# Performance work log

Hardware: AMD Instinct MI355X
Metric: run time of the kernel (lower is better)

The kernel has to match this reference:

```python
import jax, jax.numpy as jnp
import numpy as np


def _lstm_layer(x, h0, c0, W_ih, W_hh, b_ih, b_hh):
    # x: [B,T,D], h0/c0: [B,H], W_ih: [4H,D], W_hh: [4H,H]
    # Precompute input contribution for all timesteps (one big GEMM).
    xg = jnp.einsum('btd,gd->btg', x, W_ih) + (b_ih + b_hh)  # [B,T,4H]

    def step(carry, xg_t):
        h, c = carry
        g = xg_t + h @ W_hh.T  # [B,4H]
        i, f, gg, o = jnp.split(g, 4, axis=-1)  # torch gate order: i,f,g,o
        i = jax.nn.sigmoid(i)
        f = jax.nn.sigmoid(f)
        gg = jnp.tanh(gg)
        o = jax.nn.sigmoid(o)
        c = f * c + i * gg
        h = o * jnp.tanh(c)
        return (h, c), h

    (hT, cT), hs = jax.lax.scan(step, (h0, c0), jnp.swapaxes(xg, 0, 1))
    return jnp.swapaxes(hs, 0, 1), hT, cT  # [B,T,H], [B,H], [B,H]


def setup_inputs() -> dict:
    key = jax.random.key(0)
    ks = jax.random.split(key, 20)
    B, T, D, H, O = 32, 2048, 64, 256, 32
    s = 0.05
    return {
        'inputs': jax.random.normal(ks[0], (B, T, D), jnp.float32),
        'h0': jax.random.normal(ks[1], (2, B, H), jnp.float32) * s,
        'c0': jax.random.normal(ks[2], (2, B, H), jnp.float32) * s,
        'W_ih0': jax.random.normal(ks[3], (4 * H, D), jnp.float32) * s,
        'W_hh0': jax.random.normal(ks[4], (4 * H, H), jnp.float32) * s,
        'b_ih0': jax.random.normal(ks[5], (4 * H,), jnp.float32) * s,
        'b_hh0': jax.random.normal(ks[6], (4 * H,), jnp.float32) * s,
        'W_ih1': jax.random.normal(ks[7], (4 * H, H), jnp.float32) * s,
        'W_hh1': jax.random.normal(ks[8], (4 * H, H), jnp.float32) * s,
        'b_ih1': jax.random.normal(ks[9], (4 * H,), jnp.float32) * s,
        'b_hh1': jax.random.normal(ks[10], (4 * H,), jnp.float32) * s,
        'W_d0': jax.random.normal(ks[11], (H, H), jnp.float32) * s,
        'b_d0': jax.random.normal(ks[12], (H,), jnp.float32) * s,
        'W_d1': jax.random.normal(ks[13], (H, H), jnp.float32) * s,
        'b_d1': jax.random.normal(ks[14], (H,), jnp.float32) * s,
        'W_out': jax.random.normal(ks[15], (O, H), jnp.float32) * s,
        'b_out': jax.random.normal(ks[16], (O,), jnp.float32) * s,
    }


def reference(inputs, h0, c0, W_ih0, W_hh0, b_ih0, b_hh0,
              W_ih1, W_hh1, b_ih1, b_hh1,
              W_d0, b_d0, W_d1, b_d1, W_out, b_out):
    # Stacked 2-layer LSTM (batch_first) matching torch nn.LSTM.
    y0, h_0, c_0 = _lstm_layer(inputs, h0[0], c0[0], W_ih0, W_hh0, b_ih0, b_hh0)
    y1, h_1, c_1 = _lstm_layer(y0, h0[1], c0[1], W_ih1, W_hh1, b_ih1, b_hh1)
    h_n = jnp.stack([h_0, h_1], axis=0)
    c_n = jnp.stack([c_0, c_1], axis=0)
    # Dense head: two Linear+ReLU, then output Linear.
    d = jax.nn.relu(jnp.einsum('bth,oh->bto', y1, W_d0) + b_d0)
    d = jax.nn.relu(jnp.einsum('bth,oh->bto', d, W_d1) + b_d1)
    out = jnp.einsum('bth,oh->bto', d, W_out) + b_out
    return out, h_n, c_n
```

## Files before the change

kernel.cpp:

```cpp
#include <hip/hip_runtime.h>
#include <hip/hip_bf16.h>
#include <cstddef>
#include <cstdint>

#define BB 32
#define TT 2048
#define DD 64
#define HH 256
#define OO 32
#define NBLK 8

#define OUT_ELEMS (BB*TT*OO)
#define HN_OFF OUT_ELEMS
#define CN_OFF (HN_OFF + 2*BB*HH)

#define O_XBF   ((size_t)0)
#define O_H0    ((size_t)8388608)
#define O_XH1   ((size_t)41959424)
#define O_WP0   ((size_t)109101056)
#define O_WP1   ((size_t)109756416)
#define O_B0    ((size_t)110804992)
#define O_B1    ((size_t)110809088)
#define O_WD0T  ((size_t)110813184)
#define O_WD1T  ((size_t)111075328)
#define O_WOUT  ((size_t)111337472)
#define O_D0    ((size_t)111370240)
#define O_D1    (O_D0 + 256)

typedef short short8 __attribute__((ext_vector_type(8)));
typedef float f32x4 __attribute__((ext_vector_type(4)));

__device__ __forceinline__ float sigm_(float x){ return 1.0f/(1.0f+__expf(-x)); }
__device__ __forceinline__ float tanhf_(float x){
    float xc = fminf(fmaxf(x, -15.0f), 15.0f);
    float e = __expf(2.0f*xc);
    return (e-1.0f)/(e+1.0f);
}
__device__ __forceinline__ unsigned short f2bf(float f){
    __hip_bfloat16 h = __float2bfloat16(f);
    return *reinterpret_cast<unsigned short*>(&h);
}
__device__ __forceinline__ unsigned int pack2(float a, float b){
    return (unsigned int)f2bf(a) | ((unsigned int)f2bf(b) << 16);
}
__device__ __forceinline__ short8 ld8(const unsigned short* p){
    return *reinterpret_cast<const short8*>(p);
}

__device__ __forceinline__ void pollLine(const int* flags, int tgt, int lane){
    int it = 0;
    while (true) {
        int v = tgt;
        if (lane < NBLK)
            v = __hip_atomic_load(flags + lane, __ATOMIC_RELAXED, __HIP_MEMORY_SCOPE_AGENT);
        if (__all(v >= tgt)) break;
        if (++it > (1<<18)) break;
    }
    asm volatile("" ::: "memory");
}

__global__ void prep_kernel(const float* __restrict__ x, const float* __restrict__ h0,
    const float* __restrict__ Wih0, const float* __restrict__ Whh0,
    const float* __restrict__ bih0, const float* __restrict__ bhh0,
    const float* __restrict__ Wih1, const float* __restrict__ Whh1,
    const float* __restrict__ bih1, const float* __restrict__ bhh1,
    const float* __restrict__ Wd0, const float* __restrict__ Wd1,
    const float* __restrict__ Wout, char* __restrict__ ws)
{
    int i = blockIdx.x*256 + threadIdx.x;
    if (i < 4194304) {
        int t = i >> 11, rem = i & 2047, b = rem >> 6, d = rem & 63;
        ((unsigned short*)(ws+O_XBF))[i] = f2bf(x[(size_t)b*131072 + t*64 + d]);
        return;
    }
    i -= 4194304;
    if (i < 327680) {
        int R = i / 320, k = i - R*320;
        int lrow = R & 15, s = (R>>4)&1, hr = (R>>5)&3, jj = R>>7;
        int gate = 2*s + (lrow>>3);
        int h = 32*jj + 8*hr + (lrow&7);
        int src = 256*gate + h;
        float v = (k < 64) ? Wih0[src*64 + k] : Whh0[src*256 + (k-64)];
        ((unsigned short*)(ws+O_WP0))[i] = f2bf(v);
        return;
    }
    i -= 327680;
    if (i < 524288) {
        int R = i >> 9, k = i & 511;
        int lrow = R & 15, s = (R>>4)&1, hr = (R>>5)&3, jj = R>>7;
        int gate = 2*s + (lrow>>3);
        int h = 32*jj + 8*hr + (lrow&7);
        int src = 256*gate + h;
        float v = (k < 256) ? Wih1[src*256 + k] : Whh1[src*256 + (k-256)];
        ((unsigned short*)(ws+O_WP1))[i] = f2bf(v);
        return;
    }
    i -= 524288;
    if (i < 1024) { ((float*)(ws+O_B0))[i] = bih0[i] + bhh0[i]; return; }
    i -= 1024;
    if (i < 1024) { ((float*)(ws+O_B1))[i] = bih1[i] + bhh1[i]; return; }
    i -= 1024;
    if (i < 8192) { ((unsigned short*)(ws+O_H0))[i] = f2bf(h0[i]); return; }
    i -= 8192;
    if (i < 8192) {
        int b = i >> 8, h = i & 255;
        ((unsigned short*)(ws+O_XH1))[b*512 + 256 + h] = f2bf(h0[8192 + i]);
        return;
    }
    i -= 8192;
    if (i < 65536) { int o = i & 255, h = i >> 8; ((float*)(ws+O_WD0T))[i] = Wd0[o*256 + h]; return; }
    i -= 65536;
    if (i < 65536) { int o = i & 255, h = i >> 8; ((float*)(ws+O_WD1T))[i] = Wd1[o*256 + h]; return; }
    i -= 65536;
    if (i < 8192) { int o = i & 31, h = i >> 5; ((float*)(ws+O_WOUT))[i] = Wout[o*256 + h]; return; }
    i -= 8192;
    if (i < 4096) { ((int*)(ws+O_D0))[i] = 0; return; }
}

template<int L>
__device__ void lstm_body(int j, char* ws, const float* __restrict__ c0_in,
                          float* __restrict__ out)
{
    constexpr int KK  = L ? 512 : 320;
    constexpr int NKT = KK / 32;

    const int tid  = threadIdx.x;
    const int wv   = tid >> 6;
    const int lane = tid & 63;
    const int bh   = wv >> 2;
    const int hr   = wv & 3;
    const int lrow = lane & 15;
    const int q    = lane >> 4;
    const int koff = q * 8;
    const int qe   = q & 1;
    const int fb   = bh*16 + lrow;
    const int hbase= 32*j + 8*hr + 4*qe;
    const bool lo  = (lane < 32);

    const unsigned short* Wp = (const unsigned short*)(ws + (L ? O_WP1 : O_WP0));
    const float* bias = (const float*)(ws + (L ? O_B1 : O_B0));

    const int wavebase = (j*4 + hr) * 32;
    short8 a0[NKT], a1[NKT];
#pragma unroll
    for (int kk = 0; kk < NKT; ++kk) {
        a0[kk] = ld8(Wp + (size_t)(wavebase +      lrow)*KK + kk*32 + koff);
        a1[kk] = ld8(Wp + (size_t)(wavebase + 16 + lrow)*KK + kk*32 + koff);
    }

    float bi[4], bf_[4], bg[4], bo[4], c[4], hv[4];
#pragma unroll
    for (int r = 0; r < 4; ++r) {
        int hg = hbase + r;
        bi[r] = bias[hg];       bf_[r] = bias[256+hg];
        bg[r] = bias[512+hg];   bo[r]  = bias[768+hg];
        c[r]  = c0_in[(size_t)L*8192 + fb*256 + hg];
        hv[r] = 0.f;
    }

    int* flags0 = (int*)(ws + O_D0);
    int* flags1 = (int*)(ws + O_D1);
    int* myflag = (L ? flags1 : flags0) + j;

    const unsigned short* xb = (const unsigned short*)(ws + O_XBF) + fb*64  + koff;
    const unsigned short* hb = (const unsigned short*)(ws + O_H0)  + fb*256 + koff;
    const unsigned short* xh = (const unsigned short*)(ws + O_XH1) + fb*512 + koff;

    unsigned long long* stA;
    unsigned long long* stB = nullptr;
    if (L == 0) {
        stA = (unsigned long long*)((unsigned short*)(ws + O_H0)  + (size_t)8192 + fb*256 + hbase);
        stB = (unsigned long long*)((unsigned short*)(ws + O_XH1) + (size_t)fb*512 + hbase);
    } else {
        stA = (unsigned long long*)((unsigned short*)(ws + O_XH1) + (size_t)16384 + fb*512 + 256 + hbase);
    }

    for (int t = 0; t < TT; ++t) {
        f32x4 A0 = {0.f,0.f,0.f,0.f}, A1 = {0.f,0.f,0.f,0.f};

        if (L == 0) {
            short8 bx0 = ld8(xb), bx1 = ld8(xb + 32);
            A0 = __builtin_amdgcn_mfma_f32_16x16x32_bf16(a0[0], bx0, A0, 0,0,0);
            A1 = __builtin_amdgcn_mfma_f32_16x16x32_bf16(a1[0], bx0, A1, 0,0,0);
            A0 = __builtin_amdgcn_mfma_f32_16x16x32_bf16(a0[1], bx1, A0, 0,0,0);
            A1 = __builtin_amdgcn_mfma_f32_16x16x32_bf16(a1[1], bx1, A1, 0,0,0);

            pollLine(flags0, t, lane);

            short8 b[8];
#pragma unroll
            for (int kk = 0; kk < 8; ++kk) b[kk] = ld8(hb + 32*kk);
#pragma unroll
            for (int kk = 0; kk < 8; ++kk) {
                A0 = __builtin_amdgcn_mfma_f32_16x16x32_bf16(a0[2+kk], b[kk], A0, 0,0,0);
                A1 = __builtin_amdgcn_mfma_f32_16x16x32_bf16(a1[2+kk], b[kk], A1, 0,0,0);
            }
        } else {
            pollLine(flags0, t+1, lane);
            short8 b[8];
#pragma unroll
            for (int kk = 0; kk < 8; ++kk) b[kk] = ld8(xh + 32*kk);
#pragma unroll
            for (int kk = 0; kk < 8; ++kk) {
                A0 = __builtin_amdgcn_mfma_f32_16x16x32_bf16(a0[kk], b[kk], A0, 0,0,0);
                A1 = __builtin_amdgcn_mfma_f32_16x16x32_bf16(a1[kk], b[kk], A1, 0,0,0);
            }
            pollLine(flags1, t, lane);
#pragma unroll
            for (int kk = 0; kk < 8; ++kk) b[kk] = ld8(xh + 256 + 32*kk);
#pragma unroll
            for (int kk = 0; kk < 8; ++kk) {
                A0 = __builtin_amdgcn_mfma_f32_16x16x32_bf16(a0[8+kk], b[kk], A0, 0,0,0);
                A1 = __builtin_amdgcn_mfma_f32_16x16x32_bf16(a1[8+kk], b[kk], A1, 0,0,0);
            }
        }

#pragma unroll
        for (int r = 0; r < 4; ++r) {
            float x0 = A0[r], y0 = __shfl_xor(x0, 32, 64);
            float x1 = A1[r], y1 = __shfl_xor(x1, 32, 64);
            float gi = (lo ? x0 : y0) + bi[r];
            float gf = (lo ? y0 : x0) + bf_[r];
            float gg = (lo ? x1 : y1) + bg[r];
            float go = (lo ? y1 : x1) + bo[r];
            float iv = sigm_(gi), fv = sigm_(gf), gv = tanhf_(gg), ov = sigm_(go);
            c[r]  = fv*c[r] + iv*gv;
            hv[r] = ov * tanhf_(c[r]);
        }

        unsigned long long w =
            (unsigned long long)pack2(hv[0], hv[1]) |
            ((unsigned long long)pack2(hv[2], hv[3]) << 32);

        if (L == 0) {
            if (lo) __hip_atomic_store(stA, w, __ATOMIC_RELAXED, __HIP_MEMORY_SCOPE_AGENT);
            else    __hip_atomic_store(stB, w, __ATOMIC_RELAXED, __HIP_MEMORY_SCOPE_AGENT);
        } else {
            if (lo) __hip_atomic_store(stA, w, __ATOMIC_RELAXED, __HIP_MEMORY_SCOPE_AGENT);
        }

        __syncthreads();
        if (tid == 0)
            __hip_atomic_store(myflag, t+1, __ATOMIC_RELAXED, __HIP_MEMORY_SCOPE_AGENT);

        xb += 2048; hb += 8192; xh += 16384;
        stA += (L ? 4096 : 2048);
        if (L == 0) stB += 4096;
    }

    if (lo) {
#pragma unroll
        for (int r = 0; r < 4; ++r) {
            out[HN_OFF + (size_t)L*8192 + fb*256 + hbase + r] = hv[r];
            out[CN_OFF + (size_t)L*8192 + fb*256 + hbase + r] = c[r];
        }
    }
}

__global__ __launch_bounds__(512, 2) void lstm_fused(char* ws,
                                                     const float* __restrict__ c0_in,
                                                     float* __restrict__ out)
{
    if (blockIdx.x < NBLK) lstm_body<0>(blockIdx.x, ws, c0_in, out);
    else                   lstm_body<1>(blockIdx.x - NBLK, ws, c0_in, out);
}

__global__ __launch_bounds__(256) void head_kernel(const char* __restrict__ ws,
    const float* __restrict__ bd0, const float* __restrict__ bd1,
    const float* __restrict__ bout, float* __restrict__ out)
{
    const __hip_bfloat16* xh1 = (const __hip_bfloat16*)(ws + O_XH1);
    const float* Wd0T  = (const float*)(ws + O_WD0T);
    const float* Wd1T  = (const float*)(ws + O_WD1T);
    const float* WoutT = (const float*)(ws + O_WOUT);

    __shared__ float buf0[16][256];
    __shared__ float buf1[16][256];
    const int row0 = blockIdx.x * 16;
    const int tid = threadIdx.x;

#pragma unroll
    for (int i = 0; i < 16; ++i) {
        int r = row0 + i;
        int b = r >> 11, t = r & 2047;
        buf0[i][tid] = __bfloat162float(xh1[(size_t)(t+1)*16384 + b*512 + 256 + tid]);
    }
    __syncthreads();

    {
        float acc[16];
        float bv = bd0[tid];
#pragma unroll
        for (int r = 0; r < 16; ++r) acc[r] = bv;
        for (int h = 0; h < 256; ++h) {
            float w = Wd0T[h*256 + tid];
#pragma unroll
            for (int r = 0; r < 16; ++r) acc[r] += w * buf0[r][h];
        }
        __syncthreads();
#pragma unroll
        for (int r = 0; r < 16; ++r) buf1[r][tid] = fmaxf(acc[r], 0.0f);
    }
    __syncthreads();

    {
        float acc[16];
        float bv = bd1[tid];
#pragma unroll
        for (int r = 0; r < 16; ++r) acc[r] = bv;
        for (int h = 0; h < 256; ++h) {
            float w = Wd1T[h*256 + tid];
#pragma unroll
            for (int r = 0; r < 16; ++r) acc[r] += w * buf1[r][h];
        }
        __syncthreads();
#pragma unroll
        for (int r = 0; r < 16; ++r) buf0[r][tid] = fmaxf(acc[r], 0.0f);
    }
    __syncthreads();

    {
        const int o = tid & 31;
        const int rr = tid >> 5;
        float a0 = bout[o], a1 = bout[o];
        for (int h = 0; h < 256; ++h) {
            float w = WoutT[h*32 + o];
            a0 += w * buf0[rr*2 + 0][h];
            a1 += w * buf0[rr*2 + 1][h];
        }
        out[(size_t)(row0 + rr*2 + 0)*32 + o] = a0;
        out[(size_t)(row0 + rr*2 + 1)*32 + o] = a1;
    }
}

extern "C" void kernel_launch(void* const* d_in, const int* in_sizes, int n_in,
                              void* d_out, int out_size, void* d_ws, size_t ws_size,
                              hipStream_t stream) {
    const float* x    = (const float*)d_in[0];
    const float* h0   = (const float*)d_in[1];
    const float* c0   = (const float*)d_in[2];
    const float* Wih0 = (const float*)d_in[3];
    const float* Whh0 = (const float*)d_in[4];
    const float* bih0 = (const float*)d_in[5];
    const float* bhh0 = (const float*)d_in[6];
    const float* Wih1 = (const float*)d_in[7];
    const float* Whh1 = (const float*)d_in[8];
    const float* bih1 = (const float*)d_in[9];
    const float* bhh1 = (const float*)d_in[10];
    const float* Wd0  = (const float*)d_in[11];
    const float* bd0  = (const float*)d_in[12];
    const float* Wd1  = (const float*)d_in[13];
    const float* bd1  = (const float*)d_in[14];
    const float* Wout = (const float*)d_in[15];
    const float* bout = (const float*)d_in[16];

    char* ws = (char*)d_ws;
    float* out = (float*)d_out;

    prep_kernel<<<20344, 256, 0, stream>>>(x, h0, Wih0, Whh0, bih0, bhh0,
                                           Wih1, Whh1, bih1, bhh1,
                                           Wd0, Wd1, Wout, ws);
    lstm_fused<<<2*NBLK, 512, 0, stream>>>(ws, c0, out);
    head_kernel<<<4096, 256, 0, stream>>>(ws, bd0, bd1, bout, out);
}
```

Measured before the change: 12.42 ms.

## Replace per-step flag barriers with tagged hidden-state words for dataflow sync

Each hidden-state element is now stored as a 32-bit word holding the bf16 value and a timestep tag. Consumers spin on the tags of the data they actually read, so the per-step __syncthreads plus flag store/poll round trip is gone. The input x is read and converted to bf16 inside the recurrent loop, which removes the prep pass over x. The cost is double the storage and bandwidth for hidden states and a 134MB memset on every call to clear the tags.

```diff
diff --git a/kernel.cpp b/kernel.cpp
--- a/kernel.cpp
+++ b/kernel.cpp
@@ -14,21 +14,21 @@
 #define HN_OFF OUT_ELEMS
 #define CN_OFF (HN_OFF + 2*BB*HH)
 
-#define O_XBF   ((size_t)0)
-#define O_H0    ((size_t)8388608)
-#define O_XH1   ((size_t)41959424)
-#define O_WP0   ((size_t)109101056)
-#define O_WP1   ((size_t)109756416)
-#define O_B0    ((size_t)110804992)
-#define O_B1    ((size_t)110809088)
-#define O_WD0T  ((size_t)110813184)
-#define O_WD1T  ((size_t)111075328)
-#define O_WOUT  ((size_t)111337472)
-#define O_D0    ((size_t)111370240)
-#define O_D1    (O_D0 + 256)
+#define O_H0T   ((size_t)0)
+#define O_H1T   ((size_t)67141632)
+#define TAGBYTES ((size_t)134283264)
+#define O_WP0   ((size_t)134283264)
+#define O_WP1   ((size_t)134938624)
+#define O_B0    ((size_t)135987200)
+#define O_B1    ((size_t)135991296)
+#define O_WD0T  ((size_t)135995392)
+#define O_WD1T  ((size_t)136257536)
+#define O_WOUT  ((size_t)136519680)
 
 typedef short short8 __attribute__((ext_vector_type(8)));
 typedef float f32x4 __attribute__((ext_vector_type(4)));
+typedef unsigned int uint4v __attribute__((ext_vector_type(4)));
+typedef unsigned long long ull;
 
 __device__ __forceinline__ float sigm_(float x){ return 1.0f/(1.0f+__expf(-x)); }
 __device__ __forceinline__ float tanhf_(float x){
@@ -40,26 +40,59 @@
     __hip_bfloat16 h = __float2bfloat16(f);
     return *reinterpret_cast<unsigned short*>(&h);
 }
-__device__ __forceinline__ unsigned int pack2(float a, float b){
-    return (unsigned int)f2bf(a) | ((unsigned int)f2bf(b) << 16);
-}
 __device__ __forceinline__ short8 ld8(const unsigned short* p){
     return *reinterpret_cast<const short8*>(p);
 }
 
-__device__ __forceinline__ void pollLine(const int* flags, int tgt, int lane){
+__device__ __forceinline__ short8 packtile(uint4v a, uint4v b){
+    uint4v u;
+    u.x = (a.y & 0xffff0000u) | (a.x >> 16);
+    u.y = (a.w & 0xffff0000u) | (a.z >> 16);
+    u.z = (b.y & 0xffff0000u) | (b.x >> 16);
+    u.w = (b.w & 0xffff0000u) | (b.z >> 16);
+    return __builtin_bit_cast(short8, u);
+}
+__device__ __forceinline__ short8 cvt8(float4 a, float4 b){
+    uint4v u;
+    u.x = ((unsigned)f2bf(a.y)<<16) | f2bf(a.x);
+    u.y = ((unsigned)f2bf(a.w)<<16) | f2bf(a.z);
+    u.z = ((unsigned)f2bf(b.y)<<16) | f2bf(b.x);
+    u.w = ((unsigned)f2bf(b.w)<<16) | f2bf(b.z);
+    return __builtin_bit_cast(short8, u);
+}
+
+__device__ __forceinline__ void validate8(const unsigned int* base,
+                                          uint4v* va, uint4v* vb, unsigned tg)
+{
     int it = 0;
     while (true) {
-        int v = tgt;
-        if (lane < NBLK)
-            v = __hip_atomic_load(flags + lane, __ATOMIC_RELAXED, __HIP_MEMORY_SCOPE_AGENT);
-        if (__all(v >= tgt)) break;
-        if (++it > (1<<18)) break;
-    }
-    asm volatile("" ::: "memory");
-}
-
-__global__ void prep_kernel(const float* __restrict__ x, const float* __restrict__ h0,
+        unsigned bad = 0;
+#pragma unroll
+        for (int kk = 0; kk < 8; ++kk) {
+            unsigned m = ((va[kk].x ^ tg) | (va[kk].z ^ tg) |
+                          (vb[kk].x ^ tg) | (vb[kk].z ^ tg)) & 0xffffu;
+            if (m) bad |= 1u << kk;
+        }
+        if (bad == 0) return;
+#pragma unroll
+        for (int kk = 0; kk < 8; ++kk) {
+            if (bad & (1u << kk)) {
+                const ull* p = (const ull*)(base + kk*32);
+                ull u0 = __hip_atomic_load(p+0, __ATOMIC_RELAXED, __HIP_MEMORY_SCOPE_AGENT);
+                ull u1 = __hip_atomic_load(p+1, __ATOMIC_RELAXED, __HIP_MEMORY_SCOPE_AGENT);
+                ull u2 = __hip_atomic_load(p+2, __ATOMIC_RELAXED, __HIP_MEMORY_SCOPE_AGENT);
+                ull u3 = __hip_atomic_load(p+3, __ATOMIC_RELAXED, __HIP_MEMORY_SCOPE_AGENT);
+                va[kk].x = (unsigned)u0; va[kk].y = (unsigned)(u0>>32);
+                va[kk].z = (unsigned)u1; va[kk].w = (unsigned)(u1>>32);
+                vb[kk].x = (unsigned)u2; vb[kk].y = (unsigned)(u2>>32);
+                vb[kk].z = (unsigned)u3; vb[kk].w = (unsigned)(u3>>32);
+            }
+        }
+        if (++it > 4096) return;
+    }
+}
+
+__global__ void prep_kernel(const float* __restrict__ h0,
     const float* __restrict__ Wih0, const float* __restrict__ Whh0,
     const float* __restrict__ bih0, const float* __restrict__ bhh0,
     const float* __restrict__ Wih1, const float* __restrict__ Whh1,
@@ -68,12 +101,6 @@
     const float* __restrict__ Wout, char* __restrict__ ws)
 {
     int i = blockIdx.x*256 + threadIdx.x;
-    if (i < 4194304) {
-        int t = i >> 11, rem = i & 2047, b = rem >> 6, d = rem & 63;
-        ((unsigned short*)(ws+O_XBF))[i] = f2bf(x[(size_t)b*131072 + t*64 + d]);
-        return;
-    }
-    i -= 4194304;
     if (i < 327680) {
         int R = i / 320, k = i - R*320;
         int lrow = R & 15, s = (R>>4)&1, hr = (R>>5)&3, jj = R>>7;
@@ -100,11 +127,13 @@
     i -= 1024;
     if (i < 1024) { ((float*)(ws+O_B1))[i] = bih1[i] + bhh1[i]; return; }
     i -= 1024;
-    if (i < 8192) { ((unsigned short*)(ws+O_H0))[i] = f2bf(h0[i]); return; }
+    if (i < 8192) {
+        ((unsigned int*)(ws+O_H0T))[i] = ((unsigned)f2bf(h0[i])<<16) | 1u;
+        return;
+    }
     i -= 8192;
     if (i < 8192) {
-        int b = i >> 8, h = i & 255;
-        ((unsigned short*)(ws+O_XH1))[b*512 + 256 + h] = f2bf(h0[8192 + i]);
+        ((unsigned int*)(ws+O_H1T))[i] = ((unsigned)f2bf(h0[8192+i])<<16) | 1u;
         return;
     }
     i -= 8192;
@@ -113,13 +142,11 @@
     if (i < 65536) { int o = i & 255, h = i >> 8; ((float*)(ws+O_WD1T))[i] = Wd1[o*256 + h]; return; }
     i -= 65536;
     if (i < 8192) { int o = i & 31, h = i >> 5; ((float*)(ws+O_WOUT))[i] = Wout[o*256 + h]; return; }
-    i -= 8192;
-    if (i < 4096) { ((int*)(ws+O_D0))[i] = 0; return; }
 }
 
 template<int L>
-__device__ void lstm_body(int j, char* ws, const float* __restrict__ c0_in,
-                          float* __restrict__ out)
+__device__ void lstm_body(int j, char* ws, const float* __restrict__ xin,
+                          const float* __restrict__ c0_in, float* __restrict__ out)
 {
     constexpr int KK  = L ? 512 : 320;
     constexpr int NKT = KK / 32;
@@ -158,60 +185,71 @@
         hv[r] = 0.f;
     }
 
-    int* flags0 = (int*)(ws + O_D0);
-    int* flags1 = (int*)(ws + O_D1);
-    int* myflag = (L ? flags1 : flags0) + j;
-
-    const unsigned short* xb = (const unsigned short*)(ws + O_XBF) + fb*64  + koff;
-    const unsigned short* hb = (const unsigned short*)(ws + O_H0)  + fb*256 + koff;
-    const unsigned short* xh = (const unsigned short*)(ws + O_XH1) + fb*512 + koff;
-
-    unsigned long long* stA;
-    unsigned long long* stB = nullptr;
-    if (L == 0) {
-        stA = (unsigned long long*)((unsigned short*)(ws + O_H0)  + (size_t)8192 + fb*256 + hbase);
-        stB = (unsigned long long*)((unsigned short*)(ws + O_XH1) + (size_t)fb*512 + hbase);
-    } else {
-        stA = (unsigned long long*)((unsigned short*)(ws + O_XH1) + (size_t)16384 + fb*512 + 256 + hbase);
-    }
+    const unsigned int* h0t = (const unsigned int*)(ws + O_H0T);
+    const unsigned int* h1t = (const unsigned int*)(ws + O_H1T);
+    unsigned int* dst = (unsigned int*)(ws + (L ? O_H1T : O_H0T));
+    const size_t laneoff = (size_t)fb*256 + koff;
 
     for (int t = 0; t < TT; ++t) {
         f32x4 A0 = {0.f,0.f,0.f,0.f}, A1 = {0.f,0.f,0.f,0.f};
 
         if (L == 0) {
-            short8 bx0 = ld8(xb), bx1 = ld8(xb + 32);
+            const float4* xp4 = (const float4*)(xin + ((size_t)fb*TT + t)*64 + koff);
+            float4 x0 = xp4[0], x1 = xp4[1];
+            float4 x2 = xp4[8], x3 = xp4[9];
+
+            const unsigned int* hp = h0t + (size_t)t*8192 + laneoff;
+            uint4v va[8], vb[8];
+#pragma unroll
+            for (int kk = 0; kk < 8; ++kk) {
+                va[kk] = *(const uint4v*)(hp + kk*32);
+                vb[kk] = *(const uint4v*)(hp + kk*32 + 4);
+            }
+            short8 bx0 = cvt8(x0, x1), bx1 = cvt8(x2, x3);
             A0 = __builtin_amdgcn_mfma_f32_16x16x32_bf16(a0[0], bx0, A0, 0,0,0);
             A1 = __builtin_amdgcn_mfma_f32_16x16x32_bf16(a1[0], bx0, A1, 0,0,0);
             A0 = __builtin_amdgcn_mfma_f32_16x16x32_bf16(a0[1], bx1, A0, 0,0,0);
             A1 = __builtin_amdgcn_mfma_f32_16x16x32_bf16(a1[1], bx1, A1, 0,0,0);
 
-            pollLine(flags0, t, lane);
-
-            short8 b[8];
-#pragma unroll
-            for (int kk = 0; kk < 8; ++kk) b[kk] = ld8(hb + 32*kk);
+            validate8(hp, va, vb, (unsigned)(t+1));
 #pragma unroll
             for (int kk = 0; kk < 8; ++kk) {
-                A0 = __builtin_amdgcn_mfma_f32_16x16x32_bf16(a0[2+kk], b[kk], A0, 0,0,0);
-                A1 = __builtin_amdgcn_mfma_f32_16x16x32_bf16(a1[2+kk], b[kk], A1, 0,0,0);
+                short8 bfr = packtile(va[kk], vb[kk]);
+                A0 = __builtin_amdgcn_mfma_f32_16x16x32_bf16(a0[2+kk], bfr, A0, 0,0,0);
+                A1 = __builtin_amdgcn_mfma_f32_16x16x32_bf16(a1[2+kk], bfr, A1, 0,0,0);
             }
         } else {
-            pollLine(flags0, t+1, lane);
-            short8 b[8];
-#pragma unroll
-            for (int kk = 0; kk < 8; ++kk) b[kk] = ld8(xh + 32*kk);
-#pragma unroll
-            for (int kk = 0; kk < 8; ++kk) {
-                A0 = __builtin_amdgcn_mfma_f32_16x16x32_bf16(a0[kk], b[kk], A0, 0,0,0);
-                A1 = __builtin_amdgcn_mfma_f32_16x16x32_bf16(a1[kk], b[kk], A1, 0,0,0);
+            {
+                const unsigned int* ap = h0t + (size_t)(t+1)*8192 + laneoff;
+                uint4v va[8], vb[8];
+#pragma unroll
+                for (int kk = 0; kk < 8; ++kk) {
+                    va[kk] = *(const uint4v*)(ap + kk*32);
+                    vb[kk] = *(const uint4v*)(ap + kk*32 + 4);
+                }
+                validate8(ap, va, vb, (unsigned)(t+2));
+#pragma unroll
+                for (int kk = 0; kk < 8; ++kk) {
+                    short8 bfr = packtile(va[kk], vb[kk]);
+                    A0 = __builtin_amdgcn_mfma_f32_16x16x32_bf16(a0[kk], bfr, A0, 0,0,0);
+                    A1 = __builtin_amdgcn_mfma_f32_16x16x32_bf16(a1[kk], bfr, A1, 0,0,0);
+                }
             }
-            pollLine(flags1, t, lane);
-#pragma unroll
-            for (int kk = 0; kk < 8; ++kk) b[kk] = ld8(xh + 256 + 32*kk);
-#pragma unroll
-            for (int kk = 0; kk < 8; ++kk) {
-                A0 = __builtin_amdgcn_mfma_f32_16x16x32_bf16(a0[8+kk], b[kk], A0, 0,0,0);
-                A1 = __builtin_amdgcn_mfma_f32_16x16x32_bf16(a1[8+kk], b[kk], A1, 0,0,0);
+            {
+                const unsigned int* bp = h1t + (size_t)t*8192 + laneoff;
+                uint4v va[8], vb[8];
+#pragma unroll
+                for (int kk = 0; kk < 8; ++kk) {
+                    va[kk] = *(const uint4v*)(bp + kk*32);
+                    vb[kk] = *(const uint4v*)(bp + kk*32 + 4);
+                }
+                validate8(bp, va, vb, (unsigned)(t+1));
+#pragma unroll
+                for (int kk = 0; kk < 8; ++kk) {
+                    short8 bfr = packtile(va[kk], vb[kk]);
+                    A0 = __builtin_amdgcn_mfma_f32_16x16x32_bf16(a0[8+kk], bfr, A0, 0,0,0);
+                    A1 = __builtin_amdgcn_mfma_f32_16x16x32_bf16(a1[8+kk], bfr, A1, 0,0,0);
+                }
             }
         }
 
@@ -228,24 +266,18 @@
             hv[r] = ov * tanhf_(c[r]);
         }
 
-        unsigned long long w =
-            (unsigned long long)pack2(hv[0], hv[1]) |
-            ((unsigned long long)pack2(hv[2], hv[3]) << 32);
-
-        if (L == 0) {
-            if (lo) __hip_atomic_store(stA, w, __ATOMIC_RELAXED, __HIP_MEMORY_SCOPE_AGENT);
-            else    __hip_atomic_store(stB, w, __ATOMIC_RELAXED, __HIP_MEMORY_SCOPE_AGENT);
-        } else {
-            if (lo) __hip_atomic_store(stA, w, __ATOMIC_RELAXED, __HIP_MEMORY_SCOPE_AGENT);
-        }
-
-        __syncthreads();
-        if (tid == 0)
-            __hip_atomic_store(myflag, t+1, __ATOMIC_RELAXED, __HIP_MEMORY_SCOPE_AGENT);
-
-        xb += 2048; hb += 8192; xh += 16384;
-        stA += (L ? 4096 : 2048);
-        if (L == 0) stB += 4096;
+        if (lo) {
+            const unsigned tg = (unsigned)(t + 2);
+            unsigned d0 = ((unsigned)f2bf(hv[0])<<16) | tg;
+            unsigned d1 = ((unsigned)f2bf(hv[1])<<16) | tg;
+            unsigned d2 = ((unsigned)f2bf(hv[2])<<16) | tg;
+            unsigned d3 = ((unsigned)f2bf(hv[3])<<16) | tg;
+            unsigned int* dp = dst + (size_t)(t+1)*8192 + (size_t)fb*256 + hbase;
+            __hip_atomic_store((ull*)dp,     (ull)d0 | ((ull)d1<<32),
+                               __ATOMIC_RELAXED, __HIP_MEMORY_SCOPE_AGENT);
+            __hip_atomic_store((ull*)dp + 1, (ull)d2 | ((ull)d3<<32),
+                               __ATOMIC_RELAXED, __HIP_MEMORY_SCOPE_AGENT);
+        }
     }
 
     if (lo) {
@@ -258,18 +290,19 @@
 }
 
 __global__ __launch_bounds__(512, 2) void lstm_fused(char* ws,
+                                                     const float* __restrict__ xin,
                                                      const float* __restrict__ c0_in,
                                                      float* __restrict__ out)
 {
-    if (blockIdx.x < NBLK) lstm_body<0>(blockIdx.x, ws, c0_in, out);
-    else                   lstm_body<1>(blockIdx.x - NBLK, ws, c0_in, out);
+    if (blockIdx.x < NBLK) lstm_body<0>(blockIdx.x, ws, xin, c0_in, out);
+    else                   lstm_body<1>(blockIdx.x - NBLK, ws, xin, c0_in, out);
 }
 
 __global__ __launch_bounds__(256) void head_kernel(const char* __restrict__ ws,
     const float* __restrict__ bd0, const float* __restrict__ bd1,
     const float* __restrict__ bout, float* __restrict__ out)
 {
-    const __hip_bfloat16* xh1 = (const __hip_bfloat16*)(ws + O_XH1);
+    const unsigned int* h1t = (const unsigned int*)(ws + O_H1T);
     const float* Wd0T  = (const float*)(ws + O_WD0T);
     const float* Wd1T  = (const float*)(ws + O_WD1T);
     const float* WoutT = (const float*)(ws + O_WOUT);
@@ -283,7 +316,8 @@
     for (int i = 0; i < 16; ++i) {
         int r = row0 + i;
         int b = r >> 11, t = r & 2047;
-        buf0[i][tid] = __bfloat162float(xh1[(size_t)(t+1)*16384 + b*512 + 256 + tid]);
+        unsigned int d = h1t[(size_t)(t+1)*8192 + b*256 + tid];
+        buf0[i][tid] = __uint_as_float(d & 0xffff0000u);
     }
     __syncthreads();
 
@@ -357,9 +391,11 @@
     char* ws = (char*)d_ws;
     float* out = (float*)d_out;
 
-    prep_kernel<<<20344, 256, 0, stream>>>(x, h0, Wih0, Whh0, bih0, bhh0,
-                                           Wih1, Whh1, bih1, bhh1,
-                                           Wd0, Wd1, Wout, ws);
-    lstm_fused<<<2*NBLK, 512, 0, stream>>>(ws, c0, out);
+    hipMemsetAsync(ws + O_H0T, 0, TAGBYTES, stream);
+
+    prep_kernel<<<3944, 256, 0, stream>>>(h0, Wih0, Whh0, bih0, bhh0,
+                                          Wih1, Whh1, bih1, bhh1,
+                                          Wd0, Wd1, Wout, ws);
+    lstm_fused<<<2*NBLK, 512, 0, stream>>>(ws, x, c0, out);
     head_kernel<<<4096, 256, 0, stream>>>(ws, bd0, bd1, bout, out);
 }
```

New measurement: 28.17 ms. +126.8%, slower.

## Co-locate both LSTM layers in each block with layer-skewed wavefront schedule

Applied to the files above, without the earlier changes.

The recurrent kernel now runs 8 blocks instead of 16. Each block holds waves for both layers, and each wave covers all 32 batch rows across two MFMA column tiles. Layer 1 runs one step behind layer 0, and both share a single flag per block that is set through an LDS counter, so the step synchronisation drops from two poll lines to one. The bf16 transpose of x in prep is removed: x is read as fp32 and converted in registers. The goal is to cut the cross-block handshakes and prep traffic, at the cost of double the MFMA work per wave, a shared serial critical path, and a shorter poll timeout with s_sleep.

```diff
diff --git a/kernel.cpp b/kernel.cpp
--- a/kernel.cpp
+++ b/kernel.cpp
@@ -14,21 +14,21 @@
 #define HN_OFF OUT_ELEMS
 #define CN_OFF (HN_OFF + 2*BB*HH)
 
-#define O_XBF   ((size_t)0)
-#define O_H0    ((size_t)8388608)
-#define O_XH1   ((size_t)41959424)
-#define O_WP0   ((size_t)109101056)
-#define O_WP1   ((size_t)109756416)
-#define O_B0    ((size_t)110804992)
-#define O_B1    ((size_t)110809088)
-#define O_WD0T  ((size_t)110813184)
-#define O_WD1T  ((size_t)111075328)
-#define O_WOUT  ((size_t)111337472)
-#define O_D0    ((size_t)111370240)
-#define O_D1    (O_D0 + 256)
+#define O_H0B   ((size_t)0)
+#define O_H1B   ((size_t)33570816)
+#define O_WP0   ((size_t)67141632)
+#define O_WP1   ((size_t)67796992)
+#define O_B0    ((size_t)68845568)
+#define O_B1    ((size_t)68849664)
+#define O_WD0T  ((size_t)68853760)
+#define O_WD1T  ((size_t)69115904)
+#define O_WOUT  ((size_t)69378048)
+#define O_FLG   ((size_t)69410816)
 
 typedef short short8 __attribute__((ext_vector_type(8)));
 typedef float f32x4 __attribute__((ext_vector_type(4)));
+typedef unsigned int uint4v __attribute__((ext_vector_type(4)));
+typedef unsigned long long ull;
 
 __device__ __forceinline__ float sigm_(float x){ return 1.0f/(1.0f+__expf(-x)); }
 __device__ __forceinline__ float tanhf_(float x){
@@ -46,20 +46,29 @@
 __device__ __forceinline__ short8 ld8(const unsigned short* p){
     return *reinterpret_cast<const short8*>(p);
 }
-
-__device__ __forceinline__ void pollLine(const int* flags, int tgt, int lane){
+__device__ __forceinline__ short8 cvt8(float4 a, float4 b){
+    uint4v u;
+    u.x = ((unsigned)f2bf(a.y)<<16) | f2bf(a.x);
+    u.y = ((unsigned)f2bf(a.w)<<16) | f2bf(a.z);
+    u.z = ((unsigned)f2bf(b.y)<<16) | f2bf(b.x);
+    u.w = ((unsigned)f2bf(b.w)<<16) | f2bf(b.z);
+    return __builtin_bit_cast(short8, u);
+}
+
+__device__ __forceinline__ void pollFlags(const int* flags, int tgt, int lane){
     int it = 0;
     while (true) {
         int v = tgt;
         if (lane < NBLK)
             v = __hip_atomic_load(flags + lane, __ATOMIC_RELAXED, __HIP_MEMORY_SCOPE_AGENT);
         if (__all(v >= tgt)) break;
-        if (++it > (1<<18)) break;
+        __builtin_amdgcn_s_sleep(1);
+        if (++it > (1<<13)) break;
     }
     asm volatile("" ::: "memory");
 }
 
-__global__ void prep_kernel(const float* __restrict__ x, const float* __restrict__ h0,
+__global__ void prep_kernel(const float* __restrict__ h0f,
     const float* __restrict__ Wih0, const float* __restrict__ Whh0,
     const float* __restrict__ bih0, const float* __restrict__ bhh0,
     const float* __restrict__ Wih1, const float* __restrict__ Whh1,
@@ -68,12 +77,6 @@
     const float* __restrict__ Wout, char* __restrict__ ws)
 {
     int i = blockIdx.x*256 + threadIdx.x;
-    if (i < 4194304) {
-        int t = i >> 11, rem = i & 2047, b = rem >> 6, d = rem & 63;
-        ((unsigned short*)(ws+O_XBF))[i] = f2bf(x[(size_t)b*131072 + t*64 + d]);
-        return;
-    }
-    i -= 4194304;
     if (i < 327680) {
         int R = i / 320, k = i - R*320;
         int lrow = R & 15, s = (R>>4)&1, hr = (R>>5)&3, jj = R>>7;
@@ -100,13 +103,9 @@
     i -= 1024;
     if (i < 1024) { ((float*)(ws+O_B1))[i] = bih1[i] + bhh1[i]; return; }
     i -= 1024;
-    if (i < 8192) { ((unsigned short*)(ws+O_H0))[i] = f2bf(h0[i]); return; }
+    if (i < 8192) { ((unsigned short*)(ws+O_H0B))[i] = f2bf(h0f[i]); return; }
     i -= 8192;
-    if (i < 8192) {
-        int b = i >> 8, h = i & 255;
-        ((unsigned short*)(ws+O_XH1))[b*512 + 256 + h] = f2bf(h0[8192 + i]);
-        return;
-    }
+    if (i < 8192) { ((unsigned short*)(ws+O_H1B))[i] = f2bf(h0f[8192+i]); return; }
     i -= 8192;
     if (i < 65536) { int o = i & 255, h = i >> 8; ((float*)(ws+O_WD0T))[i] = Wd0[o*256 + h]; return; }
     i -= 65536;
@@ -114,162 +113,189 @@
     i -= 65536;
     if (i < 8192) { int o = i & 31, h = i >> 5; ((float*)(ws+O_WOUT))[i] = Wout[o*256 + h]; return; }
     i -= 8192;
-    if (i < 4096) { ((int*)(ws+O_D0))[i] = 0; return; }
-}
-
-template<int L>
-__device__ void lstm_body(int j, char* ws, const float* __restrict__ c0_in,
-                          float* __restrict__ out)
+    if (i < 16) { ((int*)(ws+O_FLG))[i] = 0; return; }
+}
+
+__global__ __launch_bounds__(512, 1) void lstm_fused(char* __restrict__ ws,
+                                                     const float* __restrict__ xin,
+                                                     const float* __restrict__ c0f,
+                                                     float* __restrict__ out)
 {
-    constexpr int KK  = L ? 512 : 320;
-    constexpr int NKT = KK / 32;
-
+    __shared__ int ctr[TT + 2];
+
+    const int j    = blockIdx.x;
     const int tid  = threadIdx.x;
     const int wv   = tid >> 6;
     const int lane = tid & 63;
-    const int bh   = wv >> 2;
+    const int L    = wv >> 2;
     const int hr   = wv & 3;
     const int lrow = lane & 15;
     const int q    = lane >> 4;
+    const int qe   = q & 1;
     const int koff = q * 8;
-    const int qe   = q & 1;
-    const int fb   = bh*16 + lrow;
-    const int hbase= 32*j + 8*hr + 4*qe;
-    const bool lo  = (lane < 32);
+    const bool lo  = lane < 32;
+    const int hbase = 32*j + 8*hr + 4*qe;
+
+    for (int i = tid; i < TT + 2; i += 512) ctr[i] = 0;
+    __syncthreads();
 
     const unsigned short* Wp = (const unsigned short*)(ws + (L ? O_WP1 : O_WP0));
     const float* bias = (const float*)(ws + (L ? O_B1 : O_B0));
+    unsigned short* h0b = (unsigned short*)(ws + O_H0B);
+    unsigned short* h1b = (unsigned short*)(ws + O_H1B);
+    int* flags = (int*)(ws + O_FLG);
 
     const int wavebase = (j*4 + hr) * 32;
-    short8 a0[NKT], a1[NKT];
-#pragma unroll
-    for (int kk = 0; kk < NKT; ++kk) {
-        a0[kk] = ld8(Wp + (size_t)(wavebase +      lrow)*KK + kk*32 + koff);
-        a1[kk] = ld8(Wp + (size_t)(wavebase + 16 + lrow)*KK + kk*32 + koff);
-    }
-
-    float bi[4], bf_[4], bg[4], bo[4], c[4], hv[4];
+    short8 a0[16], a1[16];
+    if (L == 0) {
+#pragma unroll
+        for (int kk = 0; kk < 10; ++kk) {
+            a0[kk] = ld8(Wp + (size_t)(wavebase +      lrow)*320 + kk*32 + koff);
+            a1[kk] = ld8(Wp + (size_t)(wavebase + 16 + lrow)*320 + kk*32 + koff);
+        }
+    } else {
+#pragma unroll
+        for (int kk = 0; kk < 16; ++kk) {
+            a0[kk] = ld8(Wp + (size_t)(wavebase +      lrow)*512 + kk*32 + koff);
+            a1[kk] = ld8(Wp + (size_t)(wavebase + 16 + lrow)*512 + kk*32 + koff);
+        }
+    }
+
+    float bI[4], bF[4], bG[4], bO[4], c[2][4], hv[2][4];
 #pragma unroll
     for (int r = 0; r < 4; ++r) {
         int hg = hbase + r;
-        bi[r] = bias[hg];       bf_[r] = bias[256+hg];
-        bg[r] = bias[512+hg];   bo[r]  = bias[768+hg];
-        c[r]  = c0_in[(size_t)L*8192 + fb*256 + hg];
-        hv[r] = 0.f;
-    }
-
-    int* flags0 = (int*)(ws + O_D0);
-    int* flags1 = (int*)(ws + O_D1);
-    int* myflag = (L ? flags1 : flags0) + j;
-
-    const unsigned short* xb = (const unsigned short*)(ws + O_XBF) + fb*64  + koff;
-    const unsigned short* hb = (const unsigned short*)(ws + O_H0)  + fb*256 + koff;
-    const unsigned short* xh = (const unsigned short*)(ws + O_XH1) + fb*512 + koff;
-
-    unsigned long long* stA;
-    unsigned long long* stB = nullptr;
-    if (L == 0) {
-        stA = (unsigned long long*)((unsigned short*)(ws + O_H0)  + (size_t)8192 + fb*256 + hbase);
-        stB = (unsigned long long*)((unsigned short*)(ws + O_XH1) + (size_t)fb*512 + hbase);
-    } else {
-        stA = (unsigned long long*)((unsigned short*)(ws + O_XH1) + (size_t)16384 + fb*512 + 256 + hbase);
-    }
-
-    for (int t = 0; t < TT; ++t) {
-        f32x4 A0 = {0.f,0.f,0.f,0.f}, A1 = {0.f,0.f,0.f,0.f};
+        bI[r] = bias[hg];      bF[r] = bias[256+hg];
+        bG[r] = bias[512+hg];  bO[r] = bias[768+hg];
+    }
+#pragma unroll
+    for (int ct = 0; ct < 2; ++ct)
+#pragma unroll
+    for (int r = 0; r < 4; ++r) {
+        c[ct][r]  = c0f[(size_t)L*8192 + (ct*16+lrow)*256 + hbase + r];
+        hv[ct][r] = 0.f;
+    }
+
+    for (int t = 0; t <= TT; ++t) {
+        float4 xf0, xf1, xf2, xf3, xf4, xf5, xf6, xf7;
+        if (L == 0 && t < TT) {
+            const float4* xA = (const float4*)(xin + ((size_t)lrow*TT + t)*64 + koff);
+            const float4* xB = (const float4*)(xin + ((size_t)(16+lrow)*TT + t)*64 + koff);
+            xf0 = xA[0]; xf1 = xA[1]; xf2 = xA[8]; xf3 = xA[9];
+            xf4 = xB[0]; xf5 = xB[1]; xf6 = xB[8]; xf7 = xB[9];
+        }
+
+        pollFlags(flags, t, lane);
+
+        bool wrote = false;
+        unsigned short* dbuf = nullptr;
+        int slot = 0;
+        f32x4 A00 = {0,0,0,0}, A01 = {0,0,0,0}, A10 = {0,0,0,0}, A11 = {0,0,0,0};
 
         if (L == 0) {
-            short8 bx0 = ld8(xb), bx1 = ld8(xb + 32);
-            A0 = __builtin_amdgcn_mfma_f32_16x16x32_bf16(a0[0], bx0, A0, 0,0,0);
-            A1 = __builtin_amdgcn_mfma_f32_16x16x32_bf16(a1[0], bx0, A1, 0,0,0);
-            A0 = __builtin_amdgcn_mfma_f32_16x16x32_bf16(a0[1], bx1, A0, 0,0,0);
-            A1 = __builtin_amdgcn_mfma_f32_16x16x32_bf16(a1[1], bx1, A1, 0,0,0);
-
-            pollLine(flags0, t, lane);
-
-            short8 b[8];
-#pragma unroll
-            for (int kk = 0; kk < 8; ++kk) b[kk] = ld8(hb + 32*kk);
-#pragma unroll
-            for (int kk = 0; kk < 8; ++kk) {
-                A0 = __builtin_amdgcn_mfma_f32_16x16x32_bf16(a0[2+kk], b[kk], A0, 0,0,0);
-                A1 = __builtin_amdgcn_mfma_f32_16x16x32_bf16(a1[2+kk], b[kk], A1, 0,0,0);
+            if (t < TT) {
+                const unsigned short* hp = h0b + (size_t)t*8192 + lrow*256 + koff;
+                short8 bx;
+                bx = cvt8(xf0, xf1);
+                A00 = __builtin_amdgcn_mfma_f32_16x16x32_bf16(a0[0], bx, A00, 0,0,0);
+                A01 = __builtin_amdgcn_mfma_f32_16x16x32_bf16(a1[0], bx, A01, 0,0,0);
+                bx = cvt8(xf2, xf3);
+                A00 = __builtin_amdgcn_mfma_f32_16x16x32_bf16(a0[1], bx, A00, 0,0,0);
+                A01 = __builtin_amdgcn_mfma_f32_16x16x32_bf16(a1[1], bx, A01, 0,0,0);
+                bx = cvt8(xf4, xf5);
+                A10 = __builtin_amdgcn_mfma_f32_16x16x32_bf16(a0[0], bx, A10, 0,0,0);
+                A11 = __builtin_amdgcn_mfma_f32_16x16x32_bf16(a1[0], bx, A11, 0,0,0);
+                bx = cvt8(xf6, xf7);
+                A10 = __builtin_amdgcn_mfma_f32_16x16x32_bf16(a0[1], bx, A10, 0,0,0);
+                A11 = __builtin_amdgcn_mfma_f32_16x16x32_bf16(a1[1], bx, A11, 0,0,0);
+#pragma unroll
+                for (int kk = 0; kk < 8; ++kk) {
+                    short8 b0 = ld8(hp + kk*32);
+                    short8 b1 = ld8(hp + 4096 + kk*32);
+                    A00 = __builtin_amdgcn_mfma_f32_16x16x32_bf16(a0[2+kk], b0, A00, 0,0,0);
+                    A01 = __builtin_amdgcn_mfma_f32_16x16x32_bf16(a1[2+kk], b0, A01, 0,0,0);
+                    A10 = __builtin_amdgcn_mfma_f32_16x16x32_bf16(a0[2+kk], b1, A10, 0,0,0);
+                    A11 = __builtin_amdgcn_mfma_f32_16x16x32_bf16(a1[2+kk], b1, A11, 0,0,0);
+                }
+                wrote = true; dbuf = h0b; slot = t + 1;
             }
         } else {
-            pollLine(flags0, t+1, lane);
-            short8 b[8];
-#pragma unroll
-            for (int kk = 0; kk < 8; ++kk) b[kk] = ld8(xh + 32*kk);
-#pragma unroll
-            for (int kk = 0; kk < 8; ++kk) {
-                A0 = __builtin_amdgcn_mfma_f32_16x16x32_bf16(a0[kk], b[kk], A0, 0,0,0);
-                A1 = __builtin_amdgcn_mfma_f32_16x16x32_bf16(a1[kk], b[kk], A1, 0,0,0);
+            if (t >= 1) {
+                const unsigned short* yp = h0b + (size_t)t*8192     + lrow*256 + koff;
+                const unsigned short* hp = h1b + (size_t)(t-1)*8192 + lrow*256 + koff;
+#pragma unroll
+                for (int kk = 0; kk < 8; ++kk) {
+                    short8 b0 = ld8(yp + kk*32);
+                    short8 b1 = ld8(yp + 4096 + kk*32);
+                    A00 = __builtin_amdgcn_mfma_f32_16x16x32_bf16(a0[kk], b0, A00, 0,0,0);
+                    A01 = __builtin_amdgcn_mfma_f32_16x16x32_bf16(a1[kk], b0, A01, 0,0,0);
+                    A10 = __builtin_amdgcn_mfma_f32_16x16x32_bf16(a0[kk], b1, A10, 0,0,0);
+                    A11 = __builtin_amdgcn_mfma_f32_16x16x32_bf16(a1[kk], b1, A11, 0,0,0);
+                }
+#pragma unroll
+                for (int kk = 0; kk < 8; ++kk) {
+                    short8 b0 = ld8(hp + kk*32);
+                    short8 b1 = ld8(hp + 4096 + kk*32);
+                    A00 = __builtin_amdgcn_mfma_f32_16x16x32_bf16(a0[8+kk], b0, A00, 0,0,0);
+                    A01 = __builtin_amdgcn_mfma_f32_16x16x32_bf16(a1[8+kk], b0, A01, 0,0,0);
+                    A10 = __builtin_amdgcn_mfma_f32_16x16x32_bf16(a0[8+kk], b1, A10, 0,0,0);
+                    A11 = __builtin_amdgcn_mfma_f32_16x16x32_bf16(a1[8+kk], b1, A11, 0,0,0);
+                }
+                wrote = true; dbuf = h1b; slot = t;
             }
-            pollLine(flags1, t, lane);
-#pragma unroll
-            for (int kk = 0; kk < 8; ++kk) b[kk] = ld8(xh + 256 + 32*kk);
-#pragma unroll
-            for (int kk = 0; kk < 8; ++kk) {
-                A0 = __builtin_amdgcn_mfma_f32_16x16x32_bf16(a0[8+kk], b[kk], A0, 0,0,0);
-                A1 = __builtin_amdgcn_mfma_f32_16x16x32_bf16(a1[8+kk], b[kk], A1, 0,0,0);
+        }
+
+        if (wrote) {
+#pragma unroll
+            for (int ct = 0; ct < 2; ++ct) {
+                f32x4 A0 = ct ? A10 : A00;
+                f32x4 A1 = ct ? A11 : A01;
+#pragma unroll
+                for (int r = 0; r < 4; ++r) {
+                    float x0 = A0[r], y0 = __shfl_xor(x0, 32, 64);
+                    float x1 = A1[r], y1 = __shfl_xor(x1, 32, 64);
+                    float gi = (lo ? x0 : y0) + bI[r];
+                    float gf = (lo ? y0 : x0) + bF[r];
+                    float gg = (lo ? x1 : y1) + bG[r];
+                    float go = (lo ? y1 : x1) + bO[r];
+                    float iv = sigm_(gi), fv = sigm_(gf), gv = tanhf_(gg), ov = sigm_(go);
+                    c[ct][r]  = fv*c[ct][r] + iv*gv;
+                    hv[ct][r] = ov * tanhf_(c[ct][r]);
+                }
+                if (lo) {
+                    ull w = (ull)pack2(hv[ct][0], hv[ct][1]) |
+                            ((ull)pack2(hv[ct][2], hv[ct][3]) << 32);
+                    ull* dp = (ull*)(dbuf + (size_t)slot*8192 + (ct*16+lrow)*256 + hbase);
+                    __hip_atomic_store(dp, w, __ATOMIC_RELAXED, __HIP_MEMORY_SCOPE_AGENT);
+                }
             }
         }
 
+        asm volatile("s_waitcnt vmcnt(0)" ::: "memory");
+        if (lane == 0) {
+            int old = atomicAdd(&ctr[t], 1);
+            if (old == 7)
+                __hip_atomic_store(flags + j, t + 1,
+                                   __ATOMIC_RELAXED, __HIP_MEMORY_SCOPE_AGENT);
+        }
+    }
+
+    if (lo) {
+#pragma unroll
+        for (int ct = 0; ct < 2; ++ct)
 #pragma unroll
         for (int r = 0; r < 4; ++r) {
-            float x0 = A0[r], y0 = __shfl_xor(x0, 32, 64);
-            float x1 = A1[r], y1 = __shfl_xor(x1, 32, 64);
-            float gi = (lo ? x0 : y0) + bi[r];
-            float gf = (lo ? y0 : x0) + bf_[r];
-            float gg = (lo ? x1 : y1) + bg[r];
-            float go = (lo ? y1 : x1) + bo[r];
-            float iv = sigm_(gi), fv = sigm_(gf), gv = tanhf_(gg), ov = sigm_(go);
-            c[r]  = fv*c[r] + iv*gv;
-            hv[r] = ov * tanhf_(c[r]);
-        }
-
-        unsigned long long w =
-            (unsigned long long)pack2(hv[0], hv[1]) |
-            ((unsigned long long)pack2(hv[2], hv[3]) << 32);
-
-        if (L == 0) {
-            if (lo) __hip_atomic_store(stA, w, __ATOMIC_RELAXED, __HIP_MEMORY_SCOPE_AGENT);
-            else    __hip_atomic_store(stB, w, __ATOMIC_RELAXED, __HIP_MEMORY_SCOPE_AGENT);
-        } else {
-            if (lo) __hip_atomic_store(stA, w, __ATOMIC_RELAXED, __HIP_MEMORY_SCOPE_AGENT);
-        }
-
-        __syncthreads();
-        if (tid == 0)
-            __hip_atomic_store(myflag, t+1, __ATOMIC_RELAXED, __HIP_MEMORY_SCOPE_AGENT);
-
-        xb += 2048; hb += 8192; xh += 16384;
-        stA += (L ? 4096 : 2048);
-        if (L == 0) stB += 4096;
-    }
-
-    if (lo) {
-#pragma unroll
-        for (int r = 0; r < 4; ++r) {
-            out[HN_OFF + (size_t)L*8192 + fb*256 + hbase + r] = hv[r];
-            out[CN_OFF + (size_t)L*8192 + fb*256 + hbase + r] = c[r];
-        }
-    }
-}
-
-__global__ __launch_bounds__(512, 2) void lstm_fused(char* ws,
-                                                     const float* __restrict__ c0_in,
-                                                     float* __restrict__ out)
-{
-    if (blockIdx.x < NBLK) lstm_body<0>(blockIdx.x, ws, c0_in, out);
-    else                   lstm_body<1>(blockIdx.x - NBLK, ws, c0_in, out);
+            out[HN_OFF + (size_t)L*8192 + (ct*16+lrow)*256 + hbase + r] = hv[ct][r];
+            out[CN_OFF + (size_t)L*8192 + (ct*16+lrow)*256 + hbase + r] = c[ct][r];
+        }
+    }
 }
 
 __global__ __launch_bounds__(256) void head_kernel(const char* __restrict__ ws,
     const float* __restrict__ bd0, const float* __restrict__ bd1,
     const float* __restrict__ bout, float* __restrict__ out)
 {
-    const __hip_bfloat16* xh1 = (const __hip_bfloat16*)(ws + O_XH1);
+    const __hip_bfloat16* h1b = (const __hip_bfloat16*)(ws + O_H1B);
     const float* Wd0T  = (const float*)(ws + O_WD0T);
     const float* Wd1T  = (const float*)(ws + O_WD1T);
     const float* WoutT = (const float*)(ws + O_WOUT);
@@ -283,7 +309,7 @@
     for (int i = 0; i < 16; ++i) {
         int r = row0 + i;
         int b = r >> 11, t = r & 2047;
-        buf0[i][tid] = __bfloat162float(xh1[(size_t)(t+1)*16384 + b*512 + 256 + tid]);
+        buf0[i][tid] = __bfloat162float(h1b[(size_t)(t+1)*8192 + b*256 + tid]);
     }
     __syncthreads();
 
@@ -357,9 +383,9 @@
     char* ws = (char*)d_ws;
     float* out = (float*)d_out;
 
-    prep_kernel<<<20344, 256, 0, stream>>>(x, h0, Wih0, Whh0, bih0, bhh0,
-                                           Wih1, Whh1, bih1, bhh1,
-                                           Wd0, Wd1, Wout, ws);
-    lstm_fused<<<2*NBLK, 512, 0, stream>>>(ws, c0, out);
+    prep_kernel<<<3945, 256, 0, stream>>>(h0, Wih0, Whh0, bih0, bhh0,
+                                          Wih1, Whh1, bih1, bhh1,
+                                          Wd0, Wd1, Wout, ws);
+    lstm_fused<<<NBLK, 512, 0, stream>>>(ws, x, c0, out);
     head_kernel<<<4096, 256, 0, stream>>>(ws, bd0, bd1, bout, out);
 }
```

Measured after the change: 19.20 ms. 1.55x slower.
